# Kernel optimization log

Measured on AMD Instinct MI355X. Metric: run time of the kernel, lower is better.

## Reference

```python
import jax, jax.numpy as jnp
import numpy as np

B, L, H, NB, D, DH = 8, 4096, 16, 8, 1024, 128

def setup_inputs() -> dict:
    key = jax.random.key(0)
    ks = jax.random.split(key, 12)
    theta_path = jax.random.normal(ks[0], (B, L, H, NB), jnp.float32)
    content_emb = jax.random.normal(ks[1], (B, L, D), jnp.float32)
    s_in = 1.0 / np.sqrt(D).astype(np.float32)
    s_h = 1.0 / np.sqrt(DH).astype(np.float32)
    # log_R_head: Linear(D,128) -> GELU -> Linear(128, H*NB), last layer weight *0.01, bias 0
    r_w1 = jax.random.normal(ks[2], (D, DH), jnp.float32) * s_in
    r_b1 = jnp.zeros((DH,), jnp.float32)
    r_w2 = jax.random.normal(ks[3], (DH, H * NB), jnp.float32) * s_h * 0.01
    r_b2 = jnp.zeros((H * NB,), jnp.float32)
    # measure_head
    m_w1 = jax.random.normal(ks[4], (D, DH), jnp.float32) * s_in
    m_b1 = jax.random.normal(ks[5], (DH,), jnp.float32) * s_in
    m_w2 = jax.random.normal(ks[6], (DH, H * NB), jnp.float32) * s_h
    m_b2 = jax.random.normal(ks[7], (H * NB,), jnp.float32) * s_h
    log_Q = jnp.full((H, NB), -3.0, jnp.float32)
    log_R_avg = jnp.full((H, NB), 1.0, jnp.float32)
    return {"theta_path": theta_path, "content_emb": content_emb,
            "log_Q": log_Q, "log_R_avg": log_R_avg,
            "r_w1": r_w1, "r_b1": r_b1, "r_w2": r_w2, "r_b2": r_b2,
            "m_w1": m_w1, "m_b1": m_b1, "m_w2": m_w2, "m_b2": m_b2}

def _mlp(x, w1, b1, w2, b2):
    h = jax.nn.gelu(x @ w1 + b1, approximate=False)  # torch nn.GELU default = exact
    return h @ w2 + b2

def reference(theta_path, content_emb, log_Q, log_R_avg,
              r_w1, r_b1, r_w2, r_b2, m_w1, m_b1, m_w2, m_b2):
    b, l, h, nb = theta_path.shape
    log_R = jnp.clip(_mlp(content_emb, r_w1, r_b1, r_w2, r_b2).reshape(b, l, h, nb), -5.0, 5.0)
    R = jnp.exp(log_R)
    z = jnp.pi * jnp.tanh(_mlp(content_emb, m_w1, m_b1, m_w2, m_b2).reshape(b, l, h, nb))
    diff = z - theta_path
    nu = jnp.arctan2(jnp.sin(diff), jnp.cos(diff))  # wrap angle error to (-pi, pi]
    Q = jnp.exp(log_Q)
    Ravg = jnp.exp(log_R_avg)
    Pi_dare = 0.5 * (-Q + jnp.sqrt(Q * Q + 4.0 * Q * Ravg))  # [H, NB]
    Pi = jnp.broadcast_to(Pi_dare[None, None], (b, l, h, nb))
    K = Pi / jnp.maximum(Pi + R, 1e-8)
    alpha = 1.0 - K
    u = K * nu
    # affine associative scan over sequence dim: d_t = alpha_t * d_{t-1} + u_t
    def combine(c1, c2):
        a1, u1 = c1
        a2, u2 = c2
        return (a2 * a1, a2 * u1 + u2)
    _, d = jax.lax.associative_scan(combine, (alpha, u), axis=1)
    return (theta_path + d, Pi, K, R)
```

## Files before the change

kernel.cpp:

```cpp
#include <hip/hip_runtime.h>
#include <hip/hip_bf16.h>
#include <cstdint>
#include <cstddef>

#define TOK 32768
#define CCH 128
#define DIN 1024

typedef __attribute__((ext_vector_type(8))) short short8;
typedef __attribute__((ext_vector_type(4))) float f32x4;

#define LIST_CAP 262144u

static __device__ __forceinline__ uint16_t f2bf(float f) {
  __hip_bfloat16 h = __float2bfloat16(f);
  return __builtin_bit_cast(uint16_t, h);
}
static __device__ __forceinline__ float bf2f(uint16_t u) {
  __hip_bfloat16 h = __builtin_bit_cast(__hip_bfloat16, u);
  return __bfloat162float(h);
}
static __device__ __forceinline__ void splitbf(float x, uint16_t& hi, uint16_t& lo) {
  hi = f2bf(x);
  lo = f2bf(x - bf2f(hi));
}

__global__ void prep_kernel(const float* __restrict__ r_w1, const float* __restrict__ r_w2,
                            const float* __restrict__ m_w1, const float* __restrict__ m_w2,
                            const float* __restrict__ logQ, const float* __restrict__ logRavg,
                            uint16_t* __restrict__ W1r, uint16_t* __restrict__ W2r,
                            uint16_t* __restrict__ W1mh, uint16_t* __restrict__ W1ml,
                            uint16_t* __restrict__ W2mh, uint16_t* __restrict__ W2ml,
                            float* __restrict__ PiArr, unsigned int* __restrict__ cnt)
{
  int idx = blockIdx.x * 256 + threadIdx.x;
  if (idx == 0) cnt[0] = 0;
  if (idx < 131072) {
    int e = idx;
    int j = e & 7, lane = (e >> 3) & 63, nt = (e >> 9) & 7, c = (e >> 12) & 1, kt = e >> 13;
    int k = kt * 64 + c * 32 + (lane >> 4) * 8 + j;
    int n = nt * 16 + (lane & 15);
    W1r[e] = f2bf(r_w1[k * 128 + n]);
  } else if (idx < 147456) {
    int e = idx - 131072;
    int j = e & 7, l = (e >> 3) & 63, c = (e >> 9) & 3, t = e >> 11;
    int k = c * 32 + (l >> 4) * 8 + j;
    int col = t * 16 + (l & 15);
    W2r[e] = f2bf(r_w2[k * 128 + col]);
  } else if (idx < 278528) {
    int e = idx - 147456;
    int j = e & 7, lane = (e >> 3) & 63, nt = (e >> 9) & 7, c = (e >> 12) & 1, kt = e >> 13;
    int k = kt * 64 + c * 32 + (lane >> 4) * 8 + j;
    int n = nt * 16 + (lane & 15);
    uint16_t h, l;
    splitbf(m_w1[k * 128 + n], h, l);
    W1mh[e] = h; W1ml[e] = l;
  } else if (idx < 294912) {
    int e = idx - 278528;
    int j = e & 7, l = (e >> 3) & 63, c = (e >> 9) & 3, t = e >> 11;
    int k = c * 32 + (l >> 4) * 8 + j;
    int col = t * 16 + (l & 15);
    uint16_t h, lo;
    splitbf(m_w2[k * 128 + col], h, lo);
    W2mh[e] = h; W2ml[e] = lo;
  } else if (idx < 295040) {
    int i = idx - 294912;
    float Q = expf(logQ[i]);
    float Rv = expf(logRavg[i]);
    PiArr[i] = 0.5f * (-Q + sqrtf(Q * Q + 4.0f * Q * Rv));
  }
}

__global__ __launch_bounds__(512, 4) void fused_all(
    const float* __restrict__ X, const float* __restrict__ theta,
    const uint16_t* __restrict__ W1r, const uint16_t* __restrict__ W2r,
    const uint16_t* __restrict__ W1h, const uint16_t* __restrict__ W1l,
    const uint16_t* __restrict__ W2h, const uint16_t* __restrict__ W2l,
    const float* __restrict__ rB1, const float* __restrict__ rB2,
    const float* __restrict__ B1, const float* __restrict__ B2,
    const float* __restrict__ PiArr,
    float* __restrict__ out0, float* __restrict__ out1,
    float* __restrict__ out2, float* __restrict__ out3,
    float* __restrict__ AggA, float* __restrict__ AggU,
    unsigned int* __restrict__ cnt, unsigned int* __restrict__ list)
{
  union SM {
    struct { uint16_t Xh[2][64][72]; uint16_t Xl[2][64][72]; } s1;
    struct { uint16_t Hh[64][136]; uint16_t Hl[64][136]; uint16_t Hr[64][136]; } s2;
    struct { float2 Agg[4][4][128]; } s3;
  };
  __shared__ SM sm;

  const int tid = threadIdx.x;
  const int w = tid >> 6, lane = tid & 63;
  const int l15 = lane & 15, l4 = lane >> 4;
  const int tm = w >> 2, tn = w & 3;
  const int tok0 = blockIdx.x * 64;

  f32x4 accm[2][2], accr[2][2];
#pragma unroll
  for (int mm = 0; mm < 2; ++mm)
#pragma unroll
    for (int t = 0; t < 2; ++t) { accm[mm][t] = 0.0f; accr[mm][t] = 0.0f; }

  const int rr = tid >> 4, cc = tid & 15;
  float4 xv0, xv1;

  auto stageLoad = [&](int kt) {
    xv0 = *reinterpret_cast<const float4*>(
        X + (size_t)(tok0 + rr) * DIN + kt * 64 + cc * 4);
    xv1 = *reinterpret_cast<const float4*>(
        X + (size_t)(tok0 + rr + 32) * DIN + kt * 64 + cc * 4);
  };
  auto stageWrite = [&](int b) {
    ushort4 vh, vl;
    splitbf(xv0.x, vh.x, vl.x);
    splitbf(xv0.y, vh.y, vl.y);
    splitbf(xv0.z, vh.z, vl.z);
    splitbf(xv0.w, vh.w, vl.w);
    *reinterpret_cast<ushort4*>(&sm.s1.Xh[b][rr][cc * 4]) = vh;
    *reinterpret_cast<ushort4*>(&sm.s1.Xl[b][rr][cc * 4]) = vl;
    splitbf(xv1.x, vh.x, vl.x);
    splitbf(xv1.y, vh.y, vl.y);
    splitbf(xv1.z, vh.z, vl.z);
    splitbf(xv1.w, vh.w, vl.w);
    *reinterpret_cast<ushort4*>(&sm.s1.Xh[b][rr + 32][cc * 4]) = vh;
    *reinterpret_cast<ushort4*>(&sm.s1.Xl[b][rr + 32][cc * 4]) = vl;
  };

  stageLoad(0);
  stageWrite(0);
  __syncthreads();

  for (int kt = 0; kt < 16; ++kt) {
    const int cur = kt & 1;
    if (kt < 15) stageLoad(kt + 1);

    short8 bh[2][2], bl[2][2], br[2][2];
#pragma unroll
    for (int c = 0; c < 2; ++c)
#pragma unroll
      for (int t = 0; t < 2; ++t) {
        const size_t boff = (size_t)((((kt * 2 + c) * 8 + (tn * 2 + t)) * 64 + lane) * 8);
        bh[c][t] = *reinterpret_cast<const short8*>(W1h + boff);
        bl[c][t] = *reinterpret_cast<const short8*>(W1l + boff);
        br[c][t] = *reinterpret_cast<const short8*>(W1r + boff);
      }

#pragma unroll
    for (int c = 0; c < 2; ++c) {
      const int ko = c * 32 + l4 * 8;
      short8 ah[2], al[2];
#pragma unroll
      for (int mm = 0; mm < 2; ++mm) {
        const int row = (tm * 2 + mm) * 16 + l15;
        ah[mm] = *reinterpret_cast<const short8*>(&sm.s1.Xh[cur][row][ko]);
        al[mm] = *reinterpret_cast<const short8*>(&sm.s1.Xl[cur][row][ko]);
      }
#pragma unroll
      for (int mm = 0; mm < 2; ++mm)
#pragma unroll
        for (int t = 0; t < 2; ++t) {
          accm[mm][t] = __builtin_amdgcn_mfma_f32_16x16x32_bf16(ah[mm], bh[c][t], accm[mm][t], 0, 0, 0);
          accm[mm][t] = __builtin_amdgcn_mfma_f32_16x16x32_bf16(al[mm], bh[c][t], accm[mm][t], 0, 0, 0);
          accm[mm][t] = __builtin_amdgcn_mfma_f32_16x16x32_bf16(ah[mm], bl[c][t], accm[mm][t], 0, 0, 0);
          accr[mm][t] = __builtin_amdgcn_mfma_f32_16x16x32_bf16(ah[mm], br[c][t], accr[mm][t], 0, 0, 0);
        }
    }

    if (kt < 15) stageWrite(cur ^ 1);
    __syncthreads();
  }

#pragma unroll
  for (int t = 0; t < 2; ++t) {
    const int n = (tn * 2 + t) * 16 + l15;
    const float b1m = B1[n];
    const float b1rr = rB1[n];
#pragma unroll
    for (int mm = 0; mm < 2; ++mm)
#pragma unroll
      for (int r = 0; r < 4; ++r) {
        const int row = (tm * 2 + mm) * 16 + l4 * 4 + r;
        const float v = accm[mm][t][r] + b1m;
        const float ev = erff(v / 1.41421356237309515f);
        const float g = 0.5f * v * (ev + 1.0f);
        uint16_t gh, gl;
        splitbf(g, gh, gl);
        sm.s2.Hh[row][n] = gh;
        sm.s2.Hl[row][n] = gl;
        const float vr = accr[mm][t][r] + b1rr;
        const float gr = 0.5f * vr * (1.0f + erff(vr * 0.70710678118654752f));
        sm.s2.Hr[row][n] = f2bf(gr);
      }
  }
  __syncthreads();

  f32x4 acc2m[2][2], acc2r[2][2];
#pragma unroll
  for (int mm = 0; mm < 2; ++mm)
#pragma unroll
    for (int t = 0; t < 2; ++t) { acc2m[mm][t] = 0.0f; acc2r[mm][t] = 0.0f; }

#pragma unroll
  for (int c2 = 0; c2 < 4; ++c2) {
    const int ko = c2 * 32 + l4 * 8;
    short8 ah[2], al[2], ar[2];
#pragma unroll
    for (int mm = 0; mm < 2; ++mm) {
      const int row = (tm * 2 + mm) * 16 + l15;
      ah[mm] = *reinterpret_cast<const short8*>(&sm.s2.Hh[row][ko]);
      al[mm] = *reinterpret_cast<const short8*>(&sm.s2.Hl[row][ko]);
      ar[mm] = *reinterpret_cast<const short8*>(&sm.s2.Hr[row][ko]);
    }
    short8 b2h[2], b2l[2], b2r[2];
#pragma unroll
    for (int t = 0; t < 2; ++t) {
      const size_t boff = (size_t)((((tn * 2 + t) * 4 + c2) * 64 + lane) * 8);
      b2h[t] = *reinterpret_cast<const short8*>(W2h + boff);
      b2l[t] = *reinterpret_cast<const short8*>(W2l + boff);
      b2r[t] = *reinterpret_cast<const short8*>(W2r + boff);
    }
#pragma unroll
    for (int mm = 0; mm < 2; ++mm)
#pragma unroll
      for (int t = 0; t < 2; ++t) {
        acc2m[mm][t] = __builtin_amdgcn_mfma_f32_16x16x32_bf16(ah[mm], b2h[t], acc2m[mm][t], 0, 0, 0);
        acc2m[mm][t] = __builtin_amdgcn_mfma_f32_16x16x32_bf16(al[mm], b2h[t], acc2m[mm][t], 0, 0, 0);
        acc2m[mm][t] = __builtin_amdgcn_mfma_f32_16x16x32_bf16(ah[mm], b2l[t], acc2m[mm][t], 0, 0, 0);
        acc2r[mm][t] = __builtin_amdgcn_mfma_f32_16x16x32_bf16(ar[mm], b2r[t], acc2r[mm][t], 0, 0, 0);
      }
  }

#pragma unroll
  for (int t = 0; t < 2; ++t) {
    const int n = (tn * 2 + t) * 16 + l15;
    const float b2 = rB2[n];
    const float piv = PiArr[n];
#pragma unroll
    for (int mm = 0; mm < 2; ++mm)
#pragma unroll
      for (int r = 0; r < 4; ++r) {
        const int token = tok0 + (tm * 2 + mm) * 16 + l4 * 4 + r;
        float lr = acc2r[mm][t][r] + b2;
        lr = fminf(fmaxf(lr, -5.0f), 5.0f);
        const float R = expf(lr);
        const float K = piv / fmaxf(piv + R, 1e-8f);
        const size_t off = (size_t)token * CCH + n;
        out1[off] = piv;
        out2[off] = K;
        out3[off] = R;
        acc2r[mm][t][r] = K;
      }
  }

#pragma unroll
  for (int t = 0; t < 2; ++t) {
    const int n = (tn * 2 + t) * 16 + l15;
    const float b2 = B2[n];
#pragma unroll
    for (int mm = 0; mm < 2; ++mm)
#pragma unroll
      for (int r = 0; r < 4; ++r) {
        const int token = tok0 + (tm * 2 + mm) * 16 + l4 * 4 + r;
        const float mz = acc2m[mm][t][r] + b2;
        const float z = 3.14159265358979323846f * tanhf(mz);
        const float d = z - theta[(size_t)token * CCH + n];
        const float wr = d - 6.2831853071795864769f * rintf(d * 0.15915494309189533577f);
        if (3.14159265358979323846f - fabsf(wr) < 3e-4f) {
          unsigned int p = atomicAdd(cnt, 1u);
          if (p < LIST_CAP) list[p] = (unsigned int)(token * CCH + n);
        }
        const float nu = atan2f(sinf(d), cosf(d));
        out0[(size_t)token * CCH + n] = nu;
        acc2m[mm][t][r] = nu;
      }
  }

  __syncthreads();
#pragma unroll
  for (int t = 0; t < 2; ++t) {
    const int n = (tn * 2 + t) * 16 + l15;
#pragma unroll
    for (int mm = 0; mm < 2; ++mm) {
      float A = 1.0f, U = 0.0f;
#pragma unroll
      for (int r = 0; r < 4; ++r) {
        const float k = acc2r[mm][t][r];
        const float v = acc2m[mm][t][r];
        const float a = 1.0f - k;
        A *= a;
        U = fmaf(a, U, k * v);
      }
      sm.s3.Agg[tm * 2 + mm][l4][n] = make_float2(A, U);
    }
  }
  __syncthreads();
  if (tid < 128) {
    const int ch = tid;
    float A = 1.0f, U = 0.0f;
#pragma unroll
    for (int g = 0; g < 16; ++g) {
      const float2 au = sm.s3.Agg[g >> 2][g & 3][ch];
      U = fmaf(au.x, U, au.y);
      A *= au.x;
    }
    AggA[blockIdx.x * CCH + ch] = A;
    AggU[blockIdx.x * CCH + ch] = U;
  }
}

__global__ __launch_bounds__(128) void refine_nu(
    const float* __restrict__ X, const float* __restrict__ theta,
    const float* __restrict__ W1, const float* __restrict__ B1,
    const float* __restrict__ W2, const float* __restrict__ B2,
    const unsigned int* __restrict__ cnt, const unsigned int* __restrict__ list,
    float* __restrict__ out0)
{
  __shared__ float h[128];
  const int j = threadIdx.x;
  const unsigned int n = min(cnt[0], LIST_CAP);
  for (unsigned int e = blockIdx.x; e < n; e += gridDim.x) {
    const unsigned int idx = list[e];
    const int tok = (int)(idx >> 7), ch = (int)(idx & 127);
    const float* xr = X + (size_t)tok * DIN;
    float acc = 0.0f;
    for (int k = 0; k < DIN; ++k)
      acc = fmaf(xr[k], W1[(size_t)k * CCH + j], acc);
    const float v = acc + B1[j];
    const float ev = erff(v / 1.41421356237309515f);
    h[j] = 0.5f * v * (ev + 1.0f);
    __syncthreads();
    if (j == 0) {
      float a2 = 0.0f;
      for (int k = 0; k < CCH; ++k)
        a2 = fmaf(h[k], W2[(size_t)k * CCH + ch], a2);
      const float mz = a2 + B2[ch];
      const float z = 3.14159265358979323846f * tanhf(mz);
      const float d = z - theta[(size_t)tok * CCH + ch];
      out0[(size_t)tok * CCH + ch] = atan2f(sinf(d), cosf(d));
    }
    __syncthreads();
  }
}

__global__ __launch_bounds__(64) void refine_agg(
    const float* __restrict__ Kk, const float* __restrict__ nu,
    const unsigned int* __restrict__ cnt, const unsigned int* __restrict__ list,
    float* __restrict__ AggA, float* __restrict__ AggU)
{
  __shared__ float av[64], uv[64];
  const int i = threadIdx.x;
  const unsigned int n = min(cnt[0], LIST_CAP);
  for (unsigned int e = blockIdx.x; e < n; e += gridDim.x) {
    const unsigned int idx = list[e];
    const int ch = (int)(idx & 127);
    const int blk = (int)(idx >> 13);
    const size_t off = (size_t)(blk * 64 + i) * CCH + ch;
    const float k = Kk[off];
    const float v = nu[off];
    av[i] = 1.0f - k;
    uv[i] = k * v;
    __syncthreads();
    if (i == 0) {
      float A = 1.0f, U = 0.0f;
      for (int g = 0; g < 64; ++g) {
        U = fmaf(av[g], U, uv[g]);
        A *= av[g];
      }
      AggA[blk * CCH + ch] = A;
      AggU[blk * CCH + ch] = U;
    }
    __syncthreads();
  }
}

__global__ __launch_bounds__(256) void scan_pass2(
    const float* __restrict__ AggA, const float* __restrict__ AggU,
    float* __restrict__ Carry)
{
  const int wid = blockIdx.x * 4 + (threadIdx.x >> 6);
  const int b = wid >> 7, ch = wid & 127;
  const int g = threadIdx.x & 63;
  const size_t idx = (size_t)(b * 64 + g) * CCH + ch;
  float A = AggA[idx];
  float U = AggU[idx];
#pragma unroll
  for (int s = 1; s < 64; s <<= 1) {
    const float pA = __shfl_up(A, s);
    const float pU = __shfl_up(U, s);
    if (g >= s) {
      U = fmaf(A, pU, U);
      A = A * pA;
    }
  }
  float cU = __shfl_up(U, 1);
  if (g == 0) cU = 0.0f;
  Carry[idx] = cU;
}

__global__ void scan_pass3(const float* __restrict__ Kk, const float* __restrict__ theta,
                           const float* __restrict__ Carry, float* __restrict__ out0)
{
  const int c = threadIdx.x;
  const int blk = blockIdx.x;
  const size_t base = (size_t)blk * 64 * CCH + c;
  float d = Carry[blk * CCH + c];
  for (int i = 0; i < 64; ++i) {
    const size_t off = base + (size_t)i * CCH;
    const float k = Kk[off];
    const float v = out0[off];
    d = fmaf(1.0f - k, d, k * v);
    out0[off] = theta[off] + d;
  }
}

extern "C" void kernel_launch(void* const* d_in, const int* in_sizes, int n_in,
                              void* d_out, int out_size, void* d_ws, size_t ws_size,
                              hipStream_t stream) {
  const float* theta   = (const float*)d_in[0];
  const float* X       = (const float*)d_in[1];
  const float* logQ    = (const float*)d_in[2];
  const float* logRavg = (const float*)d_in[3];
  const float* r_w1    = (const float*)d_in[4];
  const float* r_b1    = (const float*)d_in[5];
  const float* r_w2    = (const float*)d_in[6];
  const float* r_b2    = (const float*)d_in[7];
  const float* m_w1    = (const float*)d_in[8];
  const float* m_b1    = (const float*)d_in[9];
  const float* m_w2    = (const float*)d_in[10];
  const float* m_b2    = (const float*)d_in[11];

  float* out0 = (float*)d_out;
  float* out1 = out0 + 4194304;
  float* out2 = out0 + 2 * 4194304;
  float* out3 = out0 + 3 * 4194304;

  char* ws = (char*)d_ws;
  uint16_t* W1r  = (uint16_t*)(ws);
  uint16_t* W2r  = (uint16_t*)(ws + 262144);
  float* PiArr   = (float*)(ws + 295936);
  float* AggA    = (float*)(ws + 296448);
  float* AggU    = (float*)(ws + 558592);
  float* Carry   = (float*)(ws + 820736);
  unsigned int* cnt  = (unsigned int*)(ws + 1082880);
  unsigned int* list = (unsigned int*)(ws + 1083136);
  uint16_t* W1mh = (uint16_t*)(ws + 2131712);
  uint16_t* W1ml = (uint16_t*)(ws + 2393856);
  uint16_t* W2mh = (uint16_t*)(ws + 2656000);
  uint16_t* W2ml = (uint16_t*)(ws + 2688768);

  prep_kernel<<<1153, 256, 0, stream>>>(r_w1, r_w2, m_w1, m_w2, logQ, logRavg,
                                        W1r, W2r, W1mh, W1ml, W2mh, W2ml,
                                        PiArr, cnt);
  fused_all<<<512, 512, 0, stream>>>(X, theta, W1r, W2r, W1mh, W1ml, W2mh, W2ml,
                                     r_b1, r_b2, m_b1, m_b2, PiArr,
                                     out0, out1, out2, out3, AggA, AggU, cnt, list);
  refine_nu<<<1024, 128, 0, stream>>>(X, theta, m_w1, m_b1, m_w2, m_b2,
                                      cnt, list, out0);
  refine_agg<<<1024, 64, 0, stream>>>(out2, out0, cnt, list, AggA, AggU);
  scan_pass2<<<256, 256, 0, stream>>>(AggA, AggU, Carry);
  scan_pass3<<<512, 128, 0, stream>>>(out2, theta, Carry, out0);
}
```

Before: 134.3 us.

## Use 1024-thread blocks in fused MLP, compute wrapped angle directly, stage scan in LDS

The fused MLP kernel now runs 1024 threads per block, so each wave owns one 16-row M tile instead of two. This halves per-thread accumulators and X staging work, aiming for more waves in flight to hide latency. The atan2(sin,cos) wrap is replaced by the rint-based wrap that was already computed, with the existing near-pi refine path covering boundary cases. scan_pass3 now loads its K and nu tiles into shared memory with coalesced float4 loads before running the serial recurrence, at the cost of 64KB LDS per block.

```diff
diff --git a/kernel.cpp b/kernel.cpp
--- a/kernel.cpp
+++ b/kernel.cpp
@@ -71,7 +71,7 @@
   }
 }
 
-__global__ __launch_bounds__(512, 4) void fused_all(
+__global__ __launch_bounds__(1024, 8) void fused_all(
     const float* __restrict__ X, const float* __restrict__ theta,
     const uint16_t* __restrict__ W1r, const uint16_t* __restrict__ W2r,
     const uint16_t* __restrict__ W1h, const uint16_t* __restrict__ W1l,
@@ -97,20 +97,16 @@
   const int tm = w >> 2, tn = w & 3;
   const int tok0 = blockIdx.x * 64;
 
-  f32x4 accm[2][2], accr[2][2];
-#pragma unroll
-  for (int mm = 0; mm < 2; ++mm)
-#pragma unroll
-    for (int t = 0; t < 2; ++t) { accm[mm][t] = 0.0f; accr[mm][t] = 0.0f; }
+  f32x4 accm[2], accr[2];
+#pragma unroll
+  for (int t = 0; t < 2; ++t) { accm[t] = 0.0f; accr[t] = 0.0f; }
 
   const int rr = tid >> 4, cc = tid & 15;
-  float4 xv0, xv1;
+  float4 xv0;
 
   auto stageLoad = [&](int kt) {
     xv0 = *reinterpret_cast<const float4*>(
         X + (size_t)(tok0 + rr) * DIN + kt * 64 + cc * 4);
-    xv1 = *reinterpret_cast<const float4*>(
-        X + (size_t)(tok0 + rr + 32) * DIN + kt * 64 + cc * 4);
   };
   auto stageWrite = [&](int b) {
     ushort4 vh, vl;
@@ -120,12 +116,6 @@
     splitbf(xv0.w, vh.w, vl.w);
     *reinterpret_cast<ushort4*>(&sm.s1.Xh[b][rr][cc * 4]) = vh;
     *reinterpret_cast<ushort4*>(&sm.s1.Xl[b][rr][cc * 4]) = vl;
-    splitbf(xv1.x, vh.x, vl.x);
-    splitbf(xv1.y, vh.y, vl.y);
-    splitbf(xv1.z, vh.z, vl.z);
-    splitbf(xv1.w, vh.w, vl.w);
-    *reinterpret_cast<ushort4*>(&sm.s1.Xh[b][rr + 32][cc * 4]) = vh;
-    *reinterpret_cast<ushort4*>(&sm.s1.Xl[b][rr + 32][cc * 4]) = vl;
   };
 
   stageLoad(0);
@@ -150,22 +140,16 @@
 #pragma unroll
     for (int c = 0; c < 2; ++c) {
       const int ko = c * 32 + l4 * 8;
-      short8 ah[2], al[2];
-#pragma unroll
-      for (int mm = 0; mm < 2; ++mm) {
-        const int row = (tm * 2 + mm) * 16 + l15;
-        ah[mm] = *reinterpret_cast<const short8*>(&sm.s1.Xh[cur][row][ko]);
-        al[mm] = *reinterpret_cast<const short8*>(&sm.s1.Xl[cur][row][ko]);
+      const int row = tm * 16 + l15;
+      short8 ah = *reinterpret_cast<const short8*>(&sm.s1.Xh[cur][row][ko]);
+      short8 al = *reinterpret_cast<const short8*>(&sm.s1.Xl[cur][row][ko]);
+#pragma unroll
+      for (int t = 0; t < 2; ++t) {
+        accm[t] = __builtin_amdgcn_mfma_f32_16x16x32_bf16(ah, bh[c][t], accm[t], 0, 0, 0);
+        accm[t] = __builtin_amdgcn_mfma_f32_16x16x32_bf16(al, bh[c][t], accm[t], 0, 0, 0);
+        accm[t] = __builtin_amdgcn_mfma_f32_16x16x32_bf16(ah, bl[c][t], accm[t], 0, 0, 0);
+        accr[t] = __builtin_amdgcn_mfma_f32_16x16x32_bf16(ah, br[c][t], accr[t], 0, 0, 0);
       }
-#pragma unroll
-      for (int mm = 0; mm < 2; ++mm)
-#pragma unroll
-        for (int t = 0; t < 2; ++t) {
-          accm[mm][t] = __builtin_amdgcn_mfma_f32_16x16x32_bf16(ah[mm], bh[c][t], accm[mm][t], 0, 0, 0);
-          accm[mm][t] = __builtin_amdgcn_mfma_f32_16x16x32_bf16(al[mm], bh[c][t], accm[mm][t], 0, 0, 0);
-          accm[mm][t] = __builtin_amdgcn_mfma_f32_16x16x32_bf16(ah[mm], bl[c][t], accm[mm][t], 0, 0, 0);
-          accr[mm][t] = __builtin_amdgcn_mfma_f32_16x16x32_bf16(ah[mm], br[c][t], accr[mm][t], 0, 0, 0);
-        }
     }
 
     if (kt < 15) stageWrite(cur ^ 1);
@@ -178,41 +162,33 @@
     const float b1m = B1[n];
     const float b1rr = rB1[n];
 #pragma unroll
-    for (int mm = 0; mm < 2; ++mm)
-#pragma unroll
-      for (int r = 0; r < 4; ++r) {
-        const int row = (tm * 2 + mm) * 16 + l4 * 4 + r;
-        const float v = accm[mm][t][r] + b1m;
-        const float ev = erff(v / 1.41421356237309515f);
-        const float g = 0.5f * v * (ev + 1.0f);
-        uint16_t gh, gl;
-        splitbf(g, gh, gl);
-        sm.s2.Hh[row][n] = gh;
-        sm.s2.Hl[row][n] = gl;
-        const float vr = accr[mm][t][r] + b1rr;
-        const float gr = 0.5f * vr * (1.0f + erff(vr * 0.70710678118654752f));
-        sm.s2.Hr[row][n] = f2bf(gr);
-      }
+    for (int r = 0; r < 4; ++r) {
+      const int row = tm * 16 + l4 * 4 + r;
+      const float v = accm[t][r] + b1m;
+      const float ev = erff(v / 1.41421356237309515f);
+      const float g = 0.5f * v * (ev + 1.0f);
+      uint16_t gh, gl;
+      splitbf(g, gh, gl);
+      sm.s2.Hh[row][n] = gh;
+      sm.s2.Hl[row][n] = gl;
+      const float vr = accr[t][r] + b1rr;
+      const float gr = 0.5f * vr * (1.0f + erff(vr * 0.70710678118654752f));
+      sm.s2.Hr[row][n] = f2bf(gr);
+    }
   }
   __syncthreads();
 
-  f32x4 acc2m[2][2], acc2r[2][2];
-#pragma unroll
-  for (int mm = 0; mm < 2; ++mm)
-#pragma unroll
-    for (int t = 0; t < 2; ++t) { acc2m[mm][t] = 0.0f; acc2r[mm][t] = 0.0f; }
+  f32x4 acc2m[2], acc2r[2];
+#pragma unroll
+  for (int t = 0; t < 2; ++t) { acc2m[t] = 0.0f; acc2r[t] = 0.0f; }
 
 #pragma unroll
   for (int c2 = 0; c2 < 4; ++c2) {
     const int ko = c2 * 32 + l4 * 8;
-    short8 ah[2], al[2], ar[2];
-#pragma unroll
-    for (int mm = 0; mm < 2; ++mm) {
-      const int row = (tm * 2 + mm) * 16 + l15;
-      ah[mm] = *reinterpret_cast<const short8*>(&sm.s2.Hh[row][ko]);
-      al[mm] = *reinterpret_cast<const short8*>(&sm.s2.Hl[row][ko]);
-      ar[mm] = *reinterpret_cast<const short8*>(&sm.s2.Hr[row][ko]);
-    }
+    const int row = tm * 16 + l15;
+    short8 ah = *reinterpret_cast<const short8*>(&sm.s2.Hh[row][ko]);
+    short8 al = *reinterpret_cast<const short8*>(&sm.s2.Hl[row][ko]);
+    short8 ar = *reinterpret_cast<const short8*>(&sm.s2.Hr[row][ko]);
     short8 b2h[2], b2l[2], b2r[2];
 #pragma unroll
     for (int t = 0; t < 2; ++t) {
@@ -222,14 +198,12 @@
       b2r[t] = *reinterpret_cast<const short8*>(W2r + boff);
     }
 #pragma unroll
-    for (int mm = 0; mm < 2; ++mm)
-#pragma unroll
-      for (int t = 0; t < 2; ++t) {
-        acc2m[mm][t] = __builtin_amdgcn_mfma_f32_16x16x32_bf16(ah[mm], b2h[t], acc2m[mm][t], 0, 0, 0);
-        acc2m[mm][t] = __builtin_amdgcn_mfma_f32_16x16x32_bf16(al[mm], b2h[t], acc2m[mm][t], 0, 0, 0);
-        acc2m[mm][t] = __builtin_amdgcn_mfma_f32_16x16x32_bf16(ah[mm], b2l[t], acc2m[mm][t], 0, 0, 0);
-        acc2r[mm][t] = __builtin_amdgcn_mfma_f32_16x16x32_bf16(ar[mm], b2r[t], acc2r[mm][t], 0, 0, 0);
-      }
+    for (int t = 0; t < 2; ++t) {
+      acc2m[t] = __builtin_amdgcn_mfma_f32_16x16x32_bf16(ah, b2h[t], acc2m[t], 0, 0, 0);
+      acc2m[t] = __builtin_amdgcn_mfma_f32_16x16x32_bf16(al, b2h[t], acc2m[t], 0, 0, 0);
+      acc2m[t] = __builtin_amdgcn_mfma_f32_16x16x32_bf16(ah, b2l[t], acc2m[t], 0, 0, 0);
+      acc2r[t] = __builtin_amdgcn_mfma_f32_16x16x32_bf16(ar, b2r[t], acc2r[t], 0, 0, 0);
+    }
   }
 
 #pragma unroll
@@ -238,20 +212,18 @@
     const float b2 = rB2[n];
     const float piv = PiArr[n];
 #pragma unroll
-    for (int mm = 0; mm < 2; ++mm)
-#pragma unroll
-      for (int r = 0; r < 4; ++r) {
-        const int token = tok0 + (tm * 2 + mm) * 16 + l4 * 4 + r;
-        float lr = acc2r[mm][t][r] + b2;
-        lr = fminf(fmaxf(lr, -5.0f), 5.0f);
-        const float R = expf(lr);
-        const float K = piv / fmaxf(piv + R, 1e-8f);
-        const size_t off = (size_t)token * CCH + n;
-        out1[off] = piv;
-        out2[off] = K;
-        out3[off] = R;
-        acc2r[mm][t][r] = K;
-      }
+    for (int r = 0; r < 4; ++r) {
+      const int token = tok0 + tm * 16 + l4 * 4 + r;
+      float lr = acc2r[t][r] + b2;
+      lr = fminf(fmaxf(lr, -5.0f), 5.0f);
+      const float R = expf(lr);
+      const float K = piv / fmaxf(piv + R, 1e-8f);
+      const size_t off = (size_t)token * CCH + n;
+      out1[off] = piv;
+      out2[off] = K;
+      out3[off] = R;
+      acc2r[t][r] = K;
+    }
   }
 
 #pragma unroll
@@ -259,41 +231,35 @@
     const int n = (tn * 2 + t) * 16 + l15;
     const float b2 = B2[n];
 #pragma unroll
-    for (int mm = 0; mm < 2; ++mm)
-#pragma unroll
-      for (int r = 0; r < 4; ++r) {
-        const int token = tok0 + (tm * 2 + mm) * 16 + l4 * 4 + r;
-        const float mz = acc2m[mm][t][r] + b2;
-        const float z = 3.14159265358979323846f * tanhf(mz);
-        const float d = z - theta[(size_t)token * CCH + n];
-        const float wr = d - 6.2831853071795864769f * rintf(d * 0.15915494309189533577f);
-        if (3.14159265358979323846f - fabsf(wr) < 3e-4f) {
-          unsigned int p = atomicAdd(cnt, 1u);
-          if (p < LIST_CAP) list[p] = (unsigned int)(token * CCH + n);
-        }
-        const float nu = atan2f(sinf(d), cosf(d));
-        out0[(size_t)token * CCH + n] = nu;
-        acc2m[mm][t][r] = nu;
+    for (int r = 0; r < 4; ++r) {
+      const int token = tok0 + tm * 16 + l4 * 4 + r;
+      const float mz = acc2m[t][r] + b2;
+      const float z = 3.14159265358979323846f * tanhf(mz);
+      const float d = z - theta[(size_t)token * CCH + n];
+      const float wr = d - 6.2831853071795864769f * rintf(d * 0.15915494309189533577f);
+      if (3.14159265358979323846f - fabsf(wr) < 3e-4f) {
+        unsigned int p = atomicAdd(cnt, 1u);
+        if (p < LIST_CAP) list[p] = (unsigned int)(token * CCH + n);
       }
+      out0[(size_t)token * CCH + n] = wr;
+      acc2m[t][r] = wr;
+    }
   }
 
   __syncthreads();
 #pragma unroll
   for (int t = 0; t < 2; ++t) {
     const int n = (tn * 2 + t) * 16 + l15;
-#pragma unroll
-    for (int mm = 0; mm < 2; ++mm) {
-      float A = 1.0f, U = 0.0f;
-#pragma unroll
-      for (int r = 0; r < 4; ++r) {
-        const float k = acc2r[mm][t][r];
-        const float v = acc2m[mm][t][r];
-        const float a = 1.0f - k;
-        A *= a;
-        U = fmaf(a, U, k * v);
-      }
-      sm.s3.Agg[tm * 2 + mm][l4][n] = make_float2(A, U);
-    }
+    float A = 1.0f, U = 0.0f;
+#pragma unroll
+    for (int r = 0; r < 4; ++r) {
+      const float k = acc2r[t][r];
+      const float v = acc2m[t][r];
+      const float a = 1.0f - k;
+      A *= a;
+      U = fmaf(a, U, k * v);
+    }
+    sm.s3.Agg[tm][l4][n] = make_float2(A, U);
   }
   __syncthreads();
   if (tid < 128) {
@@ -399,18 +365,29 @@
   Carry[idx] = cU;
 }
 
-__global__ void scan_pass3(const float* __restrict__ Kk, const float* __restrict__ theta,
-                           const float* __restrict__ Carry, float* __restrict__ out0)
-{
+__global__ __launch_bounds__(128) void scan_pass3(
+    const float* __restrict__ Kk, const float* __restrict__ theta,
+    const float* __restrict__ Carry, float* __restrict__ out0)
+{
+  __shared__ float kb[64 * CCH];
+  __shared__ float vb[64 * CCH];
   const int c = threadIdx.x;
   const int blk = blockIdx.x;
-  const size_t base = (size_t)blk * 64 * CCH + c;
+  const size_t base = (size_t)blk * 64 * CCH;
+#pragma unroll
+  for (int i = 0; i < 16; ++i) {
+    const int e = i * 128 + c;
+    reinterpret_cast<float4*>(kb)[e] = reinterpret_cast<const float4*>(Kk + base)[e];
+    reinterpret_cast<float4*>(vb)[e] = reinterpret_cast<const float4*>(out0 + base)[e];
+  }
+  __syncthreads();
   float d = Carry[blk * CCH + c];
+#pragma unroll 8
   for (int i = 0; i < 64; ++i) {
-    const size_t off = base + (size_t)i * CCH;
-    const float k = Kk[off];
-    const float v = out0[off];
+    const float k = kb[i * CCH + c];
+    const float v = vb[i * CCH + c];
     d = fmaf(1.0f - k, d, k * v);
+    const size_t off = base + (size_t)i * CCH + c;
     out0[off] = theta[off] + d;
   }
 }
@@ -453,9 +430,9 @@
   prep_kernel<<<1153, 256, 0, stream>>>(r_w1, r_w2, m_w1, m_w2, logQ, logRavg,
                                         W1r, W2r, W1mh, W1ml, W2mh, W2ml,
                                         PiArr, cnt);
-  fused_all<<<512, 512, 0, stream>>>(X, theta, W1r, W2r, W1mh, W1ml, W2mh, W2ml,
-                                     r_b1, r_b2, m_b1, m_b2, PiArr,
-                                     out0, out1, out2, out3, AggA, AggU, cnt, list);
+  fused_all<<<512, 1024, 0, stream>>>(X, theta, W1r, W2r, W1mh, W1ml, W2mh, W2ml,
+                                      r_b1, r_b2, m_b1, m_b2, PiArr,
+                                      out0, out1, out2, out3, AggA, AggU, cnt, list);
   refine_nu<<<1024, 128, 0, stream>>>(X, theta, m_w1, m_b1, m_w2, m_b2,
                                       cnt, list, out0);
   refine_agg<<<1024, 64, 0, stream>>>(out2, out0, cnt, list, AggA, AggU);
```

Result: slower. 140.7 us (+4.8%).
